# Optimization experiments

Hardware: AMD Instinct MI355X
Metric: run time of the kernel (lower is better)

## Reference

```python
import jax, jax.numpy as jnp
import numpy as np

HEAD_SIZE = 64
N_EMBD = 1024
B, T = 8, 4096

def setup_inputs() -> dict:
    key = jax.random.key(0)
    k1, k2, k3, k4 = jax.random.split(key, 4)
    x = jax.random.normal(k1, (B, T, N_EMBD), dtype=jnp.float32)
    # bias-free Linear weights, stored as [in, out] so y = x @ W
    scale = 1.0 / np.sqrt(N_EMBD)
    Wk = jax.random.uniform(k2, (N_EMBD, HEAD_SIZE), jnp.float32, -scale, scale)
    Wq = jax.random.uniform(k3, (N_EMBD, HEAD_SIZE), jnp.float32, -scale, scale)
    Wv = jax.random.uniform(k4, (N_EMBD, HEAD_SIZE), jnp.float32, -scale, scale)
    return {"x": x, "Wk": Wk, "Wq": Wq, "Wv": Wv}

def reference(x, Wk, Wq, Wv):
    # x: [B, T, C]
    k = x @ Wk  # [B, T, H]
    q = x @ Wq
    v = x @ Wv
    scale = HEAD_SIZE ** -0.5
    wei = jnp.einsum('bth,bsh->bts', q, k) * scale  # [B, T, T]
    Tn = x.shape[1]
    causal = jnp.tril(jnp.ones((Tn, Tn), dtype=bool))
    wei = jnp.where(causal, wei, -jnp.inf)
    wei = jax.nn.softmax(wei, axis=-1)
    # dropout p=0.0 -> identity (eval behavior)
    out = jnp.einsum('bts,bsh->bth', wei, v)  # [B, T, H]
    return out
```

## Files before the change

### kernel.cpp

```cpp
#include <hip/hip_runtime.h>
#include <hip/hip_bf16.h>


#define HS 64
#define NE 1024
#define NB 8
#define TS 4096
#define NROW (NB * TS)

#define QKV_BUF 20480
#define QKV_XB  12288

typedef __attribute__((ext_vector_type(4)))  float f32x4;
typedef __attribute__((ext_vector_type(16))) float f32x16;
typedef __attribute__((ext_vector_type(8)))  short s16x8;
typedef __attribute__((ext_vector_type(4)))  float vfloat4;

__device__ __forceinline__ unsigned short f2bf(float x) {
  return __builtin_bit_cast(unsigned short, __float2bfloat16(x));
}
__device__ __forceinline__ unsigned pkbf(float lo, float hi) {
  return (unsigned)f2bf(lo) | ((unsigned)f2bf(hi) << 16);
}

union ABFrag { s16x8 v; unsigned d[4]; };

__device__ __forceinline__ void gl_lds16(const void* g, const unsigned char* l) {
  __builtin_amdgcn_global_load_lds(
      (const __attribute__((address_space(1))) unsigned int*)(g),
      (__attribute__((address_space(3))) unsigned int*)(l), 16, 0, 0);
}

__global__ __launch_bounds__(256) void wt_kernel(const float* __restrict__ Wk,
                                                 const float* __restrict__ Wq,
                                                 const float* __restrict__ Wv,
                                                 unsigned short* __restrict__ wT2) {
  int gid = blockIdx.x * 256 + threadIdx.x;
  int j = gid & 7;
  int t1 = gid >> 3;
  int sk = t1 % 768;
  int c  = t1 / 768;
  int g = sk / 192, n = sk % 192;
  int k = c * 32 + g * 8 + j;
  const float* W = (n < 64) ? Wq : (n < 128) ? Wk : Wv;
  float s = (n < 64) ? 0.18033688011112042f : 1.0f;
  wT2[gid] = f2bf(W[k * 64 + (n & 63)] * s);
}

__global__ __launch_bounds__(256, 4) void qkv_kernel(const float* __restrict__ x,
                                                     const unsigned short* __restrict__ wT2,
                                                     unsigned short* __restrict__ q_ws,
                                                     unsigned short* __restrict__ kf,
                                                     unsigned short* __restrict__ vf) {
  __shared__ __align__(16) unsigned char smem[2 * QKV_BUF];
  const int t = threadIdx.x;
  const int w = t >> 6, lane = t & 63;
  const int g = lane >> 4, nn = lane & 15;
  const int m0blk = blockIdx.x * 64;
  const int m0 = m0blk + w * 16;

  f32x4 acc[12];
#pragma unroll
  for (int i = 0; i < 12; ++i) acc[i] = f32x4{0.f, 0.f, 0.f, 0.f};

  const unsigned short* wsrcA = wT2 + (size_t)(w * 192 + lane) * 8;
  const int wd0 = w * 3072;
  const float* xs0 = x + (size_t)(m0blk + w * 16 + 0 + (lane >> 3)) * NE + (lane & 7) * 4;
  const float* xs1 = x + (size_t)(m0blk + w * 16 + 8 + (lane >> 3)) * NE + (lane & 7) * 4;
  const int xd0 = QKV_XB + w * 2048;
  const int xd1 = xd0 + 1024;

  const int abase = QKV_XB + (w * 16 + nn) * 128 + g * 32;
  const int wbase = (g * 192 + nn) * 16;

#define ISSUE(C)                                                               \
  {                                                                            \
    unsigned char* db_ = smem + ((C) & 1) * QKV_BUF;                           \
    gl_lds16(wsrcA + (size_t)(C) * 6144, db_ + wd0);                           \
    gl_lds16(wsrcA + (size_t)(C) * 6144 + 512, db_ + wd0 + 1024);              \
    gl_lds16(wsrcA + (size_t)(C) * 6144 + 1024, db_ + wd0 + 2048);             \
    gl_lds16(xs0 + (C) * 32, db_ + xd0);                                       \
    gl_lds16(xs1 + (C) * 32, db_ + xd1);                                       \
  }

  ISSUE(0)
  __builtin_amdgcn_sched_barrier(0);
  ISSUE(1)
  __builtin_amdgcn_sched_barrier(0);

#define PHASE(C, VM, DOISS)                                                    \
  {                                                                            \
    asm volatile("s_waitcnt vmcnt(" #VM ")" ::: "memory");                     \
    __builtin_amdgcn_s_barrier();                                              \
    __builtin_amdgcn_sched_barrier(0);                                         \
    const unsigned char* bb_ = smem + ((C) & 1) * QKV_BUF;                     \
    const vfloat4 a0_ = *(const vfloat4*)(bb_ + abase);                        \
    const vfloat4 a1_ = *(const vfloat4*)(bb_ + abase + 16);                   \
    ABFrag af;                                                                 \
    af.d[0] = pkbf(a0_.x, a0_.y); af.d[1] = pkbf(a0_.z, a0_.w);                \
    af.d[2] = pkbf(a1_.x, a1_.y); af.d[3] = pkbf(a1_.z, a1_.w);                \
    _Pragma("unroll")                                                          \
    for (int i = 0; i < 12; ++i) {                                             \
      const s16x8 bf = *(const s16x8*)(bb_ + wbase + i * 256);                 \
      acc[i] = __builtin_amdgcn_mfma_f32_16x16x32_bf16(af.v, bf, acc[i], 0, 0, 0); \
    }                                                                          \
    __builtin_amdgcn_sched_barrier(0);                                         \
    __builtin_amdgcn_s_barrier();                                              \
    __builtin_amdgcn_sched_barrier(0);                                         \
    if (DOISS) { ISSUE((C) + 2) }                                              \
    __builtin_amdgcn_sched_barrier(0);                                         \
  }

#pragma unroll
  for (int c = 0; c < 30; ++c) PHASE(c, 5, 1)
  PHASE(30, 5, 0)
  PHASE(31, 0, 0)
#undef PHASE
#undef ISSUE

  const int rbase = m0 + 4 * g;
#pragma unroll
  for (int i = 0; i < 12; ++i) {
    const int c = 16 * i + nn;
#pragma unroll
    for (int j = 0; j < 4; ++j) {
      const int rr = rbase + j;
      const unsigned short hval = f2bf(acc[i][j]);
      const int b = rr >> 12, tt = rr & 4095;
      if (c < 64) {
        q_ws[(size_t)rr * HS + c] = hval;
      } else if (c < 128) {
        const int h = c - 64;
        const size_t idx = (size_t)b * 262144 + (size_t)(tt >> 5) * 2048 +
                           (h >> 4) * 512 + ((h >> 3) & 1) * 256 +
                           (tt & 31) * 8 + (h & 7);
        kf[idx] = hval;
      } else {
        const int h = c - 128;
        const size_t idx = (size_t)b * 262144 + (size_t)(tt >> 5) * 2048 +
                           (h >> 5) * 1024 + ((tt >> 4) & 1) * 512 +
                           ((tt >> 3) & 1) * 256 + (h & 31) * 8 + (tt & 7);
        vf[idx] = hval;
      }
    }
  }
}

#define TILE32(S0, DIAG, QF, M_RUN, L_RUN, O)                                  \
  {                                                                            \
    const unsigned short* kb_ = kfb + (size_t)((S0) >> 5) * 2048 + lane * 8;   \
    const unsigned short* vb_ = vfb + (size_t)((S0) >> 5) * 2048 + lane * 8;   \
    const s16x8 ka0_ = *(const s16x8*)(kb_);                                   \
    const s16x8 ka1_ = *(const s16x8*)(kb_ + 512);                             \
    const s16x8 ka2_ = *(const s16x8*)(kb_ + 1024);                            \
    const s16x8 ka3_ = *(const s16x8*)(kb_ + 1536);                            \
    f32x16 st_;                                                                \
    _Pragma("unroll") for (int r = 0; r < 16; ++r) st_[r] = 0.f;               \
    __builtin_amdgcn_s_setprio(1);                                             \
    st_ = __builtin_amdgcn_mfma_f32_32x32x16_bf16(ka0_, QF[0], st_, 0, 0, 0);  \
    st_ = __builtin_amdgcn_mfma_f32_32x32x16_bf16(ka1_, QF[1], st_, 0, 0, 0);  \
    st_ = __builtin_amdgcn_mfma_f32_32x32x16_bf16(ka2_, QF[2], st_, 0, 0, 0);  \
    st_ = __builtin_amdgcn_mfma_f32_32x32x16_bf16(ka3_, QF[3], st_, 0, 0, 0);  \
    __builtin_amdgcn_s_setprio(0);                                             \
    if (DIAG) {                                                                \
      _Pragma("unroll") for (int r = 0; r < 16; ++r) {                         \
        const int kvl_ = (r & 3) + 8 * (r >> 2) + hi4;                         \
        if (kvl_ > qi) st_[r] = -1e30f;                                        \
      }                                                                        \
    }                                                                          \
    float mx_ =                                                                \
      fmaxf(fmaxf(fmaxf(fmaxf(st_[0], st_[1]), fmaxf(st_[2], st_[3])),         \
                  fmaxf(fmaxf(st_[4], st_[5]), fmaxf(st_[6], st_[7]))),        \
            fmaxf(fmaxf(fmaxf(st_[8], st_[9]), fmaxf(st_[10], st_[11])),       \
                  fmaxf(fmaxf(st_[12], st_[13]), fmaxf(st_[14], st_[15]))));   \
    mx_ = fmaxf(mx_, __shfl_xor(mx_, 32, 64));                                 \
    const float mn_ = fmaxf(M_RUN, mx_);                                       \
    if (__ballot(mn_ > M_RUN)) {                                               \
      const float fs_ = __builtin_amdgcn_exp2f(M_RUN - mn_);                   \
      _Pragma("unroll") for (int r = 0; r < 16; ++r) {                         \
        O[0][r] *= fs_; O[1][r] *= fs_;                                        \
      }                                                                        \
      L_RUN *= fs_;                                                            \
      M_RUN = mn_;                                                             \
    }                                                                          \
    float p_[16];                                                              \
    _Pragma("unroll") for (int r = 0; r < 16; ++r)                             \
      p_[r] = __builtin_amdgcn_exp2f(st_[r] - M_RUN);                          \
    float sm_ = ((p_[0] + p_[1]) + (p_[2] + p_[3])) +                          \
                ((p_[4] + p_[5]) + (p_[6] + p_[7]));                           \
    sm_ += ((p_[8] + p_[9]) + (p_[10] + p_[11])) +                             \
           ((p_[12] + p_[13]) + (p_[14] + p_[15]));                            \
    sm_ += __shfl_xor(sm_, 32, 64);                                            \
    L_RUN += sm_;                                                              \
    const unsigned q01_ = pkbf(p_[0], p_[1]),   q23_ = pkbf(p_[2], p_[3]);     \
    const unsigned q45_ = pkbf(p_[4], p_[5]),   q67_ = pkbf(p_[6], p_[7]);     \
    const unsigned q89_ = pkbf(p_[8], p_[9]),   qab_ = pkbf(p_[10], p_[11]);   \
    const unsigned qcd_ = pkbf(p_[12], p_[13]), qef_ = pkbf(p_[14], p_[15]);   \
    const unsigned t01_ = (unsigned)__shfl_xor((int)q01_, 32, 64);             \
    const unsigned t23_ = (unsigned)__shfl_xor((int)q23_, 32, 64);             \
    const unsigned t45_ = (unsigned)__shfl_xor((int)q45_, 32, 64);             \
    const unsigned t67_ = (unsigned)__shfl_xor((int)q67_, 32, 64);             \
    const unsigned t89_ = (unsigned)__shfl_xor((int)q89_, 32, 64);             \
    const unsigned tab_ = (unsigned)__shfl_xor((int)qab_, 32, 64);             \
    const unsigned tcd_ = (unsigned)__shfl_xor((int)qcd_, 32, 64);             \
    const unsigned tef_ = (unsigned)__shfl_xor((int)qef_, 32, 64);             \
    ABFrag pf0_, pf1_;                                                         \
    pf0_.d[0] = hi ? t45_ : q01_;                                              \
    pf0_.d[1] = hi ? t67_ : q23_;                                              \
    pf0_.d[2] = hi ? q45_ : t01_;                                              \
    pf0_.d[3] = hi ? q67_ : t23_;                                              \
    pf1_.d[0] = hi ? tcd_ : q89_;                                              \
    pf1_.d[1] = hi ? tef_ : qab_;                                              \
    pf1_.d[2] = hi ? qcd_ : t89_;                                              \
    pf1_.d[3] = hi ? qef_ : tab_;                                              \
    const s16x8 vf00_ = *(const s16x8*)(vb_);                                  \
    const s16x8 vf01_ = *(const s16x8*)(vb_ + 512);                            \
    const s16x8 vf10_ = *(const s16x8*)(vb_ + 1024);                           \
    const s16x8 vf11_ = *(const s16x8*)(vb_ + 1536);                           \
    __builtin_amdgcn_s_setprio(1);                                             \
    O[0] = __builtin_amdgcn_mfma_f32_32x32x16_bf16(vf00_, pf0_.v, O[0], 0,0,0);\
    O[0] = __builtin_amdgcn_mfma_f32_32x32x16_bf16(vf01_, pf1_.v, O[0], 0,0,0);\
    O[1] = __builtin_amdgcn_mfma_f32_32x32x16_bf16(vf10_, pf0_.v, O[1], 0,0,0);\
    O[1] = __builtin_amdgcn_mfma_f32_32x32x16_bf16(vf11_, pf1_.v, O[1], 0,0,0);\
    __builtin_amdgcn_s_setprio(0);                                             \
  }

__global__ __launch_bounds__(256, 2) void attn_kernel(const unsigned short* __restrict__ q_ws,
                                                      const unsigned short* __restrict__ kf,
                                                      const unsigned short* __restrict__ vf,
                                                      float* __restrict__ out) {
  __shared__ float o_sm[2][4][16][68];
  __shared__ float lm_sm[2][4][32][2];

  const int wv = threadIdx.x >> 6, lane = threadIdx.x & 63;
  const int qi = lane & 31, hi = lane >> 5;
  const int hi8 = 8 * hi, hi4 = 4 * hi;

  const int bid = blockIdx.x;
  const int b = bid & 7;
  const int pr = bid >> 3;
  const int tiA = pr, tiB = 127 - pr;
  const int t0A = tiA * 32, t0B = tiB * 32;

  const unsigned short* kfb = kf + (size_t)b * 262144;
  const unsigned short* vfb = vf + (size_t)b * 262144;
  const unsigned short* qrA = q_ws + (size_t)(b * TS + t0A + qi) * HS + hi8;
  const unsigned short* qrB = q_ws + (size_t)(b * TS + t0B + qi) * HS + hi8;

  s16x8 qfA[4], qfB[4];
#pragma unroll
  for (int kk = 0; kk < 4; ++kk) {
    qfA[kk] = *(const s16x8*)(qrA + 16 * kk);
    qfB[kk] = *(const s16x8*)(qrB + 16 * kk);
  }

  f32x16 oA[2], oB[2];
#pragma unroll
  for (int r = 0; r < 16; ++r) { oA[0][r] = 0.f; oA[1][r] = 0.f; oB[0][r] = 0.f; oB[1][r] = 0.f; }
  float mA = -1e30f, lA = 0.f, mB = -1e30f, lB = 0.f;

  const int ntA = tiA + 1, ntB = tiB + 1;
  for (int it = wv; it < ntB; it += 4) {
    const int s0 = it * 32;
    if (it < ntA) TILE32(s0, it == tiA, qfA, mA, lA, oA)
    TILE32(s0, it == tiB, qfB, mB, lB, oB)
  }

  if (lane < 32) {
    lm_sm[0][wv][lane][0] = mA; lm_sm[0][wv][lane][1] = lA;
    lm_sm[1][wv][lane][0] = mB; lm_sm[1][wv][lane][1] = lB;
  }
  const int q8 = (threadIdx.x >> 3) & 15;
  const int h0 = (threadIdx.x & 7) * 8;
  const int X  = threadIdx.x >> 7;
  const int t0X = X ? t0B : t0A;

#pragma unroll
  for (int P = 0; P < 2; ++P) {
    if ((qi >> 4) == P) {
      const int qr = qi & 15;
#pragma unroll
      for (int ht = 0; ht < 2; ++ht)
#pragma unroll
        for (int r = 0; r < 16; ++r) {
          const int h = ht * 32 + (r & 3) + 8 * (r >> 2) + hi4;
          o_sm[0][wv][qr][h] = oA[ht][r];
          o_sm[1][wv][qr][h] = oB[ht][r];
        }
    }
    __syncthreads();
    {
      const int q = 16 * P + q8;
      const float m0v = lm_sm[X][0][q][0], m1v = lm_sm[X][1][q][0];
      const float m2v = lm_sm[X][2][q][0], m3v = lm_sm[X][3][q][0];
      const float M = fmaxf(fmaxf(m0v, m1v), fmaxf(m2v, m3v));
      const float w0 = __builtin_amdgcn_exp2f(m0v - M);
      const float w1 = __builtin_amdgcn_exp2f(m1v - M);
      const float w2 = __builtin_amdgcn_exp2f(m2v - M);
      const float w3 = __builtin_amdgcn_exp2f(m3v - M);
      const float L = w0 * lm_sm[X][0][q][1] + w1 * lm_sm[X][1][q][1] +
                      w2 * lm_sm[X][2][q][1] + w3 * lm_sm[X][3][q][1];
      const float inv = 1.0f / L;
      float rv[8];
#pragma unroll
      for (int j = 0; j < 8; ++j)
        rv[j] = (w0 * o_sm[X][0][q8][h0 + j] + w1 * o_sm[X][1][q8][h0 + j] +
                 w2 * o_sm[X][2][q8][h0 + j] + w3 * o_sm[X][3][q8][h0 + j]) * inv;
      float* ob = out + ((size_t)(b * TS + t0X + q)) * HS + h0;
      *(float4*)(ob)     = float4{rv[0], rv[1], rv[2], rv[3]};
      *(float4*)(ob + 4) = float4{rv[4], rv[5], rv[6], rv[7]};
    }
    if (P == 0) __syncthreads();
  }
}

extern "C" void kernel_launch(void* const* d_in, const int* in_sizes, int n_in,
                              void* d_out, int out_size, void* d_ws, size_t ws_size,
                              hipStream_t stream) {
  const float* x  = (const float*)d_in[0];
  const float* Wk = (const float*)d_in[1];
  const float* Wq = (const float*)d_in[2];
  const float* Wv = (const float*)d_in[3];
  float* out = (float*)d_out;

  unsigned short* wT2  = (unsigned short*)d_ws;
  unsigned short* q_ws = wT2 + 192 * 1024;
  unsigned short* kf   = q_ws + (size_t)NROW * HS;
  unsigned short* vf   = kf + (size_t)NROW * HS;

  wt_kernel<<<dim3(768), dim3(256), 0, stream>>>(Wk, Wq, Wv, wT2);
  qkv_kernel<<<dim3(NROW / 64), dim3(256), 0, stream>>>(x, wT2, q_ws, kf, vf);
  attn_kernel<<<dim3(512), dim3(256), 0, stream>>>(q_ws, kf, vf, out);
}
```

Measured before the change: 70.56 us.

## Software-prefetch next K tiles and issue V loads ahead of compute

Restructures the attention inner loop so K fragments for the next iteration are loaded into registers while the current tile computes, and V fragments are issued at the start of each iteration before the QK MFMAs. The goal is to hide global-memory latency behind MFMA and softmax work. It also loads redundant tiles (index 0) for inactive A streams, and it raises VGPR pressure under a 2-waves-per-SIMD launch bound, which risks spills.

```diff
diff --git a/kernel.cpp b/kernel.cpp
--- a/kernel.cpp
+++ b/kernel.cpp
@@ -146,21 +146,15 @@
   }
 }
 
-#define TILE32(S0, DIAG, QF, M_RUN, L_RUN, O)                                  \
+#define TILE32F(DIAG, KF, VF, QF, M_RUN, L_RUN, O)                             \
   {                                                                            \
-    const unsigned short* kb_ = kfb + (size_t)((S0) >> 5) * 2048 + lane * 8;   \
-    const unsigned short* vb_ = vfb + (size_t)((S0) >> 5) * 2048 + lane * 8;   \
-    const s16x8 ka0_ = *(const s16x8*)(kb_);                                   \
-    const s16x8 ka1_ = *(const s16x8*)(kb_ + 512);                             \
-    const s16x8 ka2_ = *(const s16x8*)(kb_ + 1024);                            \
-    const s16x8 ka3_ = *(const s16x8*)(kb_ + 1536);                            \
     f32x16 st_;                                                                \
     _Pragma("unroll") for (int r = 0; r < 16; ++r) st_[r] = 0.f;               \
     __builtin_amdgcn_s_setprio(1);                                             \
-    st_ = __builtin_amdgcn_mfma_f32_32x32x16_bf16(ka0_, QF[0], st_, 0, 0, 0);  \
-    st_ = __builtin_amdgcn_mfma_f32_32x32x16_bf16(ka1_, QF[1], st_, 0, 0, 0);  \
-    st_ = __builtin_amdgcn_mfma_f32_32x32x16_bf16(ka2_, QF[2], st_, 0, 0, 0);  \
-    st_ = __builtin_amdgcn_mfma_f32_32x32x16_bf16(ka3_, QF[3], st_, 0, 0, 0);  \
+    st_ = __builtin_amdgcn_mfma_f32_32x32x16_bf16(KF[0], QF[0], st_, 0, 0, 0); \
+    st_ = __builtin_amdgcn_mfma_f32_32x32x16_bf16(KF[1], QF[1], st_, 0, 0, 0); \
+    st_ = __builtin_amdgcn_mfma_f32_32x32x16_bf16(KF[2], QF[2], st_, 0, 0, 0); \
+    st_ = __builtin_amdgcn_mfma_f32_32x32x16_bf16(KF[3], QF[3], st_, 0, 0, 0); \
     __builtin_amdgcn_s_setprio(0);                                             \
     if (DIAG) {                                                                \
       _Pragma("unroll") for (int r = 0; r < 16; ++r) {                         \
@@ -213,17 +207,19 @@
     pf1_.d[1] = hi ? tef_ : qab_;                                              \
     pf1_.d[2] = hi ? qcd_ : t89_;                                              \
     pf1_.d[3] = hi ? qef_ : tab_;                                              \
-    const s16x8 vf00_ = *(const s16x8*)(vb_);                                  \
-    const s16x8 vf01_ = *(const s16x8*)(vb_ + 512);                            \
-    const s16x8 vf10_ = *(const s16x8*)(vb_ + 1024);                           \
-    const s16x8 vf11_ = *(const s16x8*)(vb_ + 1536);                           \
     __builtin_amdgcn_s_setprio(1);                                             \
-    O[0] = __builtin_amdgcn_mfma_f32_32x32x16_bf16(vf00_, pf0_.v, O[0], 0,0,0);\
-    O[0] = __builtin_amdgcn_mfma_f32_32x32x16_bf16(vf01_, pf1_.v, O[0], 0,0,0);\
-    O[1] = __builtin_amdgcn_mfma_f32_32x32x16_bf16(vf10_, pf0_.v, O[1], 0,0,0);\
-    O[1] = __builtin_amdgcn_mfma_f32_32x32x16_bf16(vf11_, pf1_.v, O[1], 0,0,0);\
+    O[0] = __builtin_amdgcn_mfma_f32_32x32x16_bf16(VF[0], pf0_.v, O[0], 0,0,0);\
+    O[0] = __builtin_amdgcn_mfma_f32_32x32x16_bf16(VF[1], pf1_.v, O[0], 0,0,0);\
+    O[1] = __builtin_amdgcn_mfma_f32_32x32x16_bf16(VF[2], pf0_.v, O[1], 0,0,0);\
+    O[1] = __builtin_amdgcn_mfma_f32_32x32x16_bf16(VF[3], pf1_.v, O[1], 0,0,0);\
     __builtin_amdgcn_s_setprio(0);                                             \
   }
+
+#define LD4(dst, base)                                                         \
+  dst[0] = *(const s16x8*)(base);                                              \
+  dst[1] = *(const s16x8*)((base) + 512);                                      \
+  dst[2] = *(const s16x8*)((base) + 1024);                                     \
+  dst[3] = *(const s16x8*)((base) + 1536);
 
 __global__ __launch_bounds__(256, 2) void attn_kernel(const unsigned short* __restrict__ q_ws,
                                                       const unsigned short* __restrict__ kf,
@@ -242,8 +238,8 @@
   const int tiA = pr, tiB = 127 - pr;
   const int t0A = tiA * 32, t0B = tiB * 32;
 
-  const unsigned short* kfb = kf + (size_t)b * 262144;
-  const unsigned short* vfb = vf + (size_t)b * 262144;
+  const unsigned short* kfb = kf + (size_t)b * 262144 + lane * 8;
+  const unsigned short* vfb = vf + (size_t)b * 262144 + lane * 8;
   const unsigned short* qrA = q_ws + (size_t)(b * TS + t0A + qi) * HS + hi8;
   const unsigned short* qrB = q_ws + (size_t)(b * TS + t0B + qi) * HS + hi8;
 
@@ -260,10 +256,26 @@
   float mA = -1e30f, lA = 0.f, mB = -1e30f, lB = 0.f;
 
   const int ntA = tiA + 1, ntB = tiB + 1;
+
+  s16x8 kA[4], kB[4];
+  LD4(kA, kfb + (size_t)((wv < ntA) ? wv : 0) * 2048)
+  LD4(kB, kfb + (size_t)wv * 2048)
+
   for (int it = wv; it < ntB; it += 4) {
-    const int s0 = it * 32;
-    if (it < ntA) TILE32(s0, it == tiA, qfA, mA, lA, oA)
-    TILE32(s0, it == tiB, qfB, mB, lB, oB)
+    const bool dA = it < ntA;
+    const int nxt = it + 4;
+    s16x8 vA[4], vB[4];
+    LD4(vA, vfb + (size_t)(dA ? it : 0) * 2048)
+    LD4(vB, vfb + (size_t)it * 2048)
+    s16x8 kAn[4], kBn[4];
+    LD4(kAn, kfb + (size_t)((nxt < ntA) ? nxt : 0) * 2048)
+    LD4(kBn, kfb + (size_t)((nxt < ntB) ? nxt : 0) * 2048)
+
+    if (dA) TILE32F(it == tiA, kA, vA, qfA, mA, lA, oA)
+    TILE32F(it == tiB, kB, vB, qfB, mB, lB, oB)
+
+#pragma unroll
+    for (int kk = 0; kk < 4; ++kk) { kA[kk] = kAn[kk]; kB[kk] = kBn[kk]; }
   }
 
   if (lane < 32) {
```

After: 70.98 us. About the same (+0.6%).
